# Performance work log

Measured on AMD Instinct MI355X. Metric: run time of the kernel, lower is better.

## Reference

```python
import jax, jax.numpy as jnp
import numpy as np

N_SRC, N_DST = 1000, 1000
N = N_SRC + N_DST          # 2000 == feat_in of SW MLP (hard-coded in original)
D = 128                    # metapath2vec embedding dim
H = 256                    # SW hidden width
B = 100000                 # skip-gram (center, context) pairs
K = 5                      # negatives per pair
EP = 200000                # positive-graph edges
EN = 200000                # negative-graph edges


def setup_inputs() -> dict:
    key = jax.random.key(0)
    ks = jax.random.split(key, 12)
    node_embed = jax.random.normal(ks[0], (N, D), jnp.float32) * 0.1
    context_embed = jax.random.normal(ks[1], (N, D), jnp.float32) * 0.1
    # symmetric bipartite adjacency: etype plus its reverse asetype, homogenized
    A = (jax.random.uniform(ks[2], (N_SRC, N_DST)) < 0.02).astype(jnp.float32)
    adj = jnp.block([[jnp.zeros((N_SRC, N_SRC), jnp.float32), A],
                     [A.T, jnp.zeros((N_DST, N_DST), jnp.float32)]])
    W1 = jax.random.normal(ks[3], (N, H), jnp.float32) / np.sqrt(N).astype(np.float32)
    b1 = jnp.zeros((H,), jnp.float32)
    W2 = jax.random.normal(ks[4], (H, D), jnp.float32) / np.sqrt(H).astype(np.float32)
    b2 = jnp.zeros((D,), jnp.float32)
    pos_u = jax.random.randint(ks[5], (B,), 0, N)
    pos_v = jax.random.randint(ks[6], (B,), 0, N)
    neg_v = jax.random.randint(ks[7], (B, K), 0, N)
    pos_src = jax.random.randint(ks[8], (EP,), 0, N_SRC)
    pos_dst = jax.random.randint(ks[9], (EP,), 0, N_DST)
    neg_src = jax.random.randint(ks[10], (EN,), 0, N_SRC)
    neg_dst = jax.random.randint(ks[11], (EN,), 0, N_DST)
    return dict(node_embed=node_embed, context_embed=context_embed, adj=adj,
                W1=W1, b1=b1, W2=W2, b2=b2,
                pos_u=pos_u, pos_v=pos_v, neg_v=neg_v,
                pos_src=pos_src, pos_dst=pos_dst,
                neg_src=neg_src, neg_dst=neg_dst)


def _skipgram_loss(node_embed, context_embed, pos_u, pos_v, neg_v):
    # DGL MetaPath2Vec negative-sampling skip-gram loss
    emb_u = node_embed[pos_u]            # [B, D] gather
    emb_v = context_embed[pos_v]         # [B, D] gather
    pos = jnp.clip(jnp.sum(emb_u * emb_v, axis=-1), -10.0, 10.0)
    pos_loss = -jax.nn.log_sigmoid(pos)
    emb_neg = context_embed[neg_v]       # [B, K, D] gather
    neg = jnp.clip(jnp.einsum('bkd,bd->bk', emb_neg, emb_u), -10.0, 10.0)
    neg_loss = -jnp.sum(jax.nn.log_sigmoid(-neg), axis=-1)
    return jnp.mean(pos_loss + neg_loss)


def _sw_embedding(adj, feats, W1, b1, W2, b2):
    # adj @ adj @ adj * adj  /  outer(diag(adj@adj))  -> L2-row-normalized -> MLP
    A2 = adj @ adj                       # [N, N]
    part1 = (A2 @ adj) * adj             # 3-path counts masked onto existing edges
    d = jnp.diag(A2)                     # [N]
    part2 = d[:, None] * d[None, :]      # outer product of 2-path counts
    ok = part2 > 0
    gamma = jnp.where(ok, part1 / jnp.where(ok, part2, 1.0), 0.0)  # == nan_to_num
    norm = jnp.sqrt(jnp.sum(gamma * gamma, axis=-1, keepdims=True))
    gamma = gamma / jnp.maximum(norm, 1e-12)          # F.normalize(p=2, dim=1)
    sw_h = jnp.tanh(gamma @ W1 + b1) @ W2 + b2        # [N, 128]
    return jnp.concatenate([feats, sw_h], axis=1)     # [N, 256]


def reference(node_embed, context_embed, adj, W1, b1, W2, b2,
              pos_u, pos_v, neg_v, pos_src, pos_dst, neg_src, neg_dst):
    loss = _skipgram_loss(node_embed, context_embed, pos_u, pos_v, neg_v)
    # feats[etype[0]] ++ feats[etype[2]] == full node_embed table in global order
    h = _sw_embedding(adj, node_embed, W1, b1, W2, b2)
    h_src, h_dst = h[:N_SRC], h[N_SRC:]
    # HeteroDotPredictor: u_dot_v per edge -> [E, 1]
    pos_score = jnp.sum(h_src[pos_src] * h_dst[pos_dst], axis=-1, keepdims=True)
    neg_score = jnp.sum(h_src[neg_src] * h_dst[neg_dst], axis=-1, keepdims=True)
    return loss, pos_score, neg_score
```

## Files before the change

### kernel.cpp

```cpp
#include <hip/hip_runtime.h>
#include <hip/hip_bf16.h>

typedef __attribute__((ext_vector_type(8))) short bf16x8;
typedef __attribute__((ext_vector_type(4))) float f32x4;
typedef __attribute__((ext_vector_type(4))) unsigned short u16x4;
typedef unsigned short u16;

#define BATCH 100000
#define EPE 200000

#define OFF_AP    ((size_t)0)
#define OFF_ATP   ((size_t)2097152)
#define OFF_SP    ((size_t)4194304)
#define OFF_T1    ((size_t)6291456)
#define OFF_G     ((size_t)6291456)
#define OFF_GT    ((size_t)10485760)
#define OFF_GNS   ((size_t)14680064)
#define OFF_GNDT  ((size_t)16777216)
#define OFF_W1AT  ((size_t)18874368)
#define OFF_W1BT  ((size_t)19398656)
#define OFF_W2T   ((size_t)19922944)
#define OFF_HID   ((size_t)19988480)
#define OFF_NEP   ((size_t)21037056)
#define OFF_CEP   ((size_t)21561344)
#define OFF_HSRC  ((size_t)22085632)
#define OFF_HDST  ((size_t)22609920)
#define OFF_T2    ((size_t)23134208)
#define OFF_DEGS  ((size_t)27328512)
#define OFF_DEGD  ((size_t)27332608)
#define OFF_PART  ((size_t)27336704)

__device__ __forceinline__ u16 f2b(float f) {
  union { float f; unsigned u; } v; v.f = f;
  unsigned r = v.u + 0x7fffu + ((v.u >> 16) & 1u);
  return (u16)(r >> 16);
}
__device__ __forceinline__ float b2f(u16 h) {
  union { unsigned u; float f; } v; v.u = ((unsigned)h) << 16;
  return v.f;
}

#define AS1C(p) ((const __attribute__((address_space(1))) void*)(p))
#define AS3(p)  ((__attribute__((address_space(3))) void*)(p))

__global__ __launch_bounds__(256) void prep(const float* __restrict__ adj,
    const float* __restrict__ W1, const float* __restrict__ W2,
    const float* __restrict__ ne, const float* __restrict__ ce,
    u16* __restrict__ Ap, u16* __restrict__ ATp,
    u16* __restrict__ W1At, u16* __restrict__ W1Bt, u16* __restrict__ w2t,
    u16* __restrict__ nep, u16* __restrict__ cep,
    u16* __restrict__ hsrcp, u16* __restrict__ hdstp,
    float* __restrict__ degd, float* __restrict__ degs) {
  __shared__ float tile[64][65];
  __shared__ float redf[256];
  __shared__ float4 red4[8][32];
  int b = blockIdx.x;
  int t = threadIdx.x;
  int tx = t & 63, ty = t >> 6;
  if (b < 256) {
    int tr = b >> 4, tc = b & 15;
    int l16 = t & 15, rq = t >> 4;
    #pragma unroll
    for (int p = 0; p < 4; p++) {
      int r = p * 16 + rq;
      int gr = tr * 64 + r, gc0 = tc * 64 + l16 * 4;
      float4 v = {0.f, 0.f, 0.f, 0.f};
      if (gr < 1000 && gc0 < 1000) v = *(const float4*)&adj[(size_t)gr * 2000 + 1000 + gc0];
      u16x4 pk = {f2b(v.x), f2b(v.y), f2b(v.z), f2b(v.w)};
      *(u16x4*)&Ap[(size_t)gr * 1024 + gc0] = pk;
      tile[r][l16 * 4 + 0] = v.x;
      tile[r][l16 * 4 + 1] = v.y;
      tile[r][l16 * 4 + 2] = v.z;
      tile[r][l16 * 4 + 3] = v.w;
    }
    __syncthreads();
    #pragma unroll
    for (int p = 0; p < 16; p++) {
      int r = p * 4 + ty;
      ATp[(size_t)(tc * 64 + r) * 1024 + tr * 64 + tx] = f2b(tile[tx][r]);
    }
  } else if (b < 384) {
    int b2 = b - 256;
    int half = b2 >> 6, rem = b2 & 63;
    int jt = rem >> 2, ht = rem & 3;
    #pragma unroll
    for (int p = 0; p < 16; p++) {
      int r = p * 4 + ty;
      int j = jt * 64 + r;
      tile[r][tx] = (j < 1000) ? W1[(size_t)(half * 1000 + j) * 256 + ht * 64 + tx] : 0.f;
    }
    __syncthreads();
    u16* outp = half ? W1Bt : W1At;
    #pragma unroll
    for (int p = 0; p < 16; p++) {
      int r = p * 4 + ty;
      outp[(size_t)(ht * 64 + r) * 1024 + jt * 64 + tx] = f2b(tile[tx][r]);
    }
  } else if (b < 392) {
    int b3 = b - 384;
    int dt = b3 >> 2, kt = b3 & 3;
    #pragma unroll
    for (int p = 0; p < 16; p++) {
      int r = p * 4 + ty;
      tile[r][tx] = W2[(size_t)(kt * 64 + r) * 128 + dt * 64 + tx];
    }
    __syncthreads();
    #pragma unroll
    for (int p = 0; p < 16; p++) {
      int r = p * 4 + ty;
      w2t[(size_t)(dt * 64 + r) * 256 + kt * 64 + tx] = f2b(tile[tx][r]);
    }
  } else if (b < 648) {
    int idx = (b - 392) * 256 + t;
    int i = idx >> 5, d4 = (idx & 31) * 4;
    float4 nv = {0.f, 0.f, 0.f, 0.f}, cv = {0.f, 0.f, 0.f, 0.f};
    if (i < 2000) {
      nv = *(const float4*)&ne[(size_t)i * 128 + d4];
      cv = *(const float4*)&ce[(size_t)i * 128 + d4];
    }
    u16x4 nb = {f2b(nv.x), f2b(nv.y), f2b(nv.z), f2b(nv.w)};
    u16x4 cb = {f2b(cv.x), f2b(cv.y), f2b(cv.z), f2b(cv.w)};
    u16x4 zz = {0, 0, 0, 0};
    *(u16x4*)&nep[(size_t)i * 128 + d4] = nb;
    *(u16x4*)&cep[(size_t)i * 128 + d4] = cb;
    if (i < 1000)                   *(u16x4*)&hsrcp[(size_t)i * 256 + d4] = nb;
    else if (i < 1024)              *(u16x4*)&hsrcp[(size_t)i * 256 + d4] = zz;
    if (i >= 1000 && i < 2000)      *(u16x4*)&hdstp[(size_t)(i - 1000) * 256 + d4] = nb;
    else if (i >= 2000 && i < 2024) *(u16x4*)&hdstp[(size_t)(i - 1000) * 256 + d4] = zz;
  } else if (b < 656) {
    int jb = b - 648;
    int cx = t & 31, ry = t >> 5;
    int j4 = jb * 128 + cx * 4;
    float4 s = {0.f, 0.f, 0.f, 0.f};
    if (j4 < 1000)
      for (int i = ry; i < 1000; i += 8) {
        float4 v = *(const float4*)&adj[(size_t)i * 2000 + 1000 + j4];
        s.x += v.x; s.y += v.y; s.z += v.z; s.w += v.w;
      }
    red4[ry][cx] = s;
    __syncthreads();
    if (ry == 0) {
      float4 tot = {0.f, 0.f, 0.f, 0.f};
      #pragma unroll
      for (int k = 0; k < 8; k++) {
        float4 v = red4[k][cx];
        tot.x += v.x; tot.y += v.y; tot.z += v.z; tot.w += v.w;
      }
      *(float4*)&degd[j4] = tot;
    }
  } else {
    int ib = b - 656;
    int r = t >> 3, c8 = t & 7;
    int i = ib * 32 + r;
    float s = 0.f;
    if (i < 1000)
      for (int k4 = c8 * 4; k4 < 1000; k4 += 32) {
        float4 v = *(const float4*)&adj[(size_t)i * 2000 + 1000 + k4];
        s += v.x + v.y + v.z + v.w;
      }
    redf[t] = s;
    __syncthreads();
    if (c8 == 0) {
      float tot = 0.f;
      #pragma unroll
      for (int k = 0; k < 8; k++) tot += redf[r * 8 + k];
      degs[i] = (i < 1000) ? tot : 0.f;
    }
  }
}

__device__ __forceinline__ f32x4 gemm_core32(const u16* __restrict__ A, const u16* __restrict__ BT,
    int K, int lda, int ldbt, int brow, int bcol, u16* As, u16* Bs) {
  const int t = threadIdx.x;
  const int w = t >> 6, lane = t & 63;
  const int wr = w >> 1, wc = w & 1;
  const int r16 = lane & 15, kg = lane >> 4;
  const int row = t >> 3, cc = t & 7;
  f32x4 acc = {0.f, 0.f, 0.f, 0.f};
  const int nst = K >> 6;
  {
    const u16* ga = A + (size_t)(brow + row) * lda + cc * 8;
    __builtin_amdgcn_global_load_lds(AS1C(ga), AS3(As + t * 8), 16, 0, 0);
    const u16* gb = BT + (size_t)(bcol + row) * ldbt + cc * 8;
    __builtin_amdgcn_global_load_lds(AS1C(gb), AS3(Bs + t * 8), 16, 0, 0);
  }
  int cur = 0;
  for (int s = 0; s < nst; ++s) {
    __syncthreads();
    if (s + 1 < nst) {
      int k0 = (s + 1) << 6, nb = cur ^ 1;
      const u16* ga = A + (size_t)(brow + row) * lda + k0 + cc * 8;
      __builtin_amdgcn_global_load_lds(AS1C(ga), AS3(As + nb * 2048 + t * 8), 16, 0, 0);
      const u16* gb = BT + (size_t)(bcol + row) * ldbt + k0 + cc * 8;
      __builtin_amdgcn_global_load_lds(AS1C(gb), AS3(Bs + nb * 2048 + t * 8), 16, 0, 0);
    }
    const u16* Asc = As + cur * 2048;
    const u16* Bsc = Bs + cur * 2048;
    #pragma unroll
    for (int kk = 0; kk < 2; ++kk) {
      bf16x8 af = *(const bf16x8*)&Asc[(wr * 16 + r16) * 64 + kk * 32 + kg * 8];
      bf16x8 bf_ = *(const bf16x8*)&Bsc[(wc * 16 + r16) * 64 + kk * 32 + kg * 8];
      acc = __builtin_amdgcn_mfma_f32_16x16x32_bf16(af, bf_, acc, 0, 0, 0);
    }
    cur ^= 1;
  }
  return acc;
}

__global__ __launch_bounds__(256) void mega1(const u16* __restrict__ nep, const u16* __restrict__ cep,
    const u16* __restrict__ Ap, u16* __restrict__ T1, u16* __restrict__ Sp) {
  __shared__ u16 As[2 * 2048];
  __shared__ u16 Bs[2 * 2048];
  __shared__ u16 mir[32][33];
  int b = blockIdx.x;
  const int t = threadIdx.x;
  const int w = t >> 6, lane = t & 63;
  const int wr = w >> 1, wc = w & 1;
  const int r16 = lane & 15, kg = lane >> 4;
  if (b < 4096) {
    int brow = (b >> 6) * 32, bcol = (b & 63) * 32;
    f32x4 acc = gemm_core32(nep, cep, 128, 128, 128, brow, bcol, As, Bs);
    #pragma unroll
    for (int j = 0; j < 4; j++) {
      int row = brow + wr * 16 + kg * 4 + j, col = bcol + wc * 16 + r16;
      T1[(size_t)row * 2048 + col] = f2b(acc[j]);
    }
  } else {
    int s = b - 4096;
    int bi = (int)((sqrtf(8.f * s + 1.f) - 1.f) * 0.5f);
    while (bi * (bi + 1) / 2 > s) bi--;
    while ((bi + 1) * (bi + 2) / 2 <= s) bi++;
    int bj = s - bi * (bi + 1) / 2;
    int brow = bi * 32, bcol = bj * 32;
    f32x4 acc = gemm_core32(Ap, Ap, 1024, 1024, 1024, brow, bcol, As, Bs);
    #pragma unroll
    for (int j = 0; j < 4; j++) {
      int lr = wr * 16 + kg * 4 + j, lc = wc * 16 + r16;
      u16 v = f2b(acc[j]);
      Sp[(size_t)(brow + lr) * 1024 + bcol + lc] = v;
      mir[lr][lc] = v;
    }
    __syncthreads();
    #pragma unroll
    for (int p = 0; p < 4; p++) {
      int idx = p * 256 + t, rr = idx >> 5, cc2 = idx & 31;
      Sp[(size_t)(bcol + rr) * 1024 + brow + cc2] = mir[cc2][rr];
    }
  }
}

__global__ __launch_bounds__(256) void mega2(const u16* __restrict__ Sp, const u16* __restrict__ ATp,
    const u16* __restrict__ Ap, const float* __restrict__ degs, const float* __restrict__ degd,
    float* __restrict__ G, float* __restrict__ Gt,
    const u16* __restrict__ T1, const int* __restrict__ pu, const int* __restrict__ pv,
    const int* __restrict__ nv, float* __restrict__ partial) {
  __shared__ u16 As[2 * 2048];
  __shared__ u16 Bs[2 * 2048];
  __shared__ float gtile[32][33];
  __shared__ float red[256];
  int b = blockIdx.x;
  const int t = threadIdx.x;
  if (b >= 1024) {
    int s = (b - 1024) * 256 + t;
    float loss = 0.f;
    if (s < BATCH) {
      const u16* trow = T1 + (size_t)pu[s] * 2048;
      const int* nvb = nv + (size_t)s * 5;
      float ap = b2f(trow[pv[s]]);
      ap = fminf(fmaxf(ap, -10.f), 10.f); loss = log1pf(expf(-ap));
      #pragma unroll
      for (int k = 0; k < 5; k++) {
        float a = b2f(trow[nvb[k]]);
        a = fminf(fmaxf(a, -10.f), 10.f);
        loss += log1pf(expf(a));
      }
    }
    red[t] = loss;
    __syncthreads();
    for (int off = 128; off > 0; off >>= 1) {
      if (t < off) red[t] += red[t + off];
      __syncthreads();
    }
    if (t == 0) partial[b - 1024] = red[0];
    return;
  }
  const int w = t >> 6, lane = t & 63;
  const int wr = w >> 1, wc = w & 1;
  const int r16 = lane & 15, kg = lane >> 4;
  int brow = (b >> 5) * 32, bcol = (b & 31) * 32;
  f32x4 acc = gemm_core32(Sp, ATp, 1024, 1024, 1024, brow, bcol, As, Bs);
  #pragma unroll
  for (int j = 0; j < 4; j++) {
    int lr = wr * 16 + kg * 4 + j, lc = wc * 16 + r16;
    int row = brow + lr, col = bcol + lc;
    float a = b2f(Ap[(size_t)row * 1024 + col]);
    float p2 = degs[row] * degd[col];
    float g = (p2 > 0.f) ? (acc[j] * a) / p2 : 0.f;
    G[(size_t)row * 1024 + col] = g;
    gtile[lr][lc] = g;
  }
  __syncthreads();
  #pragma unroll
  for (int p = 0; p < 4; p++) {
    int idx = p * 256 + t, rr = idx >> 5, cc2 = idx & 31;
    Gt[(size_t)(bcol + rr) * 1024 + brow + cc2] = gtile[cc2][rr];
  }
}

template <int EPI>
__global__ __launch_bounds__(256) void gemm_bt(
    const u16* __restrict__ A, const u16* __restrict__ BT,
    const u16* __restrict__ A2, const u16* __restrict__ BT2,
    int K, int lda, int ldbt,
    u16* __restrict__ outb,
    float* __restrict__ outf, int ldo,
    const float* __restrict__ bias,
    u16* __restrict__ hsrcp, u16* __restrict__ hdstp)
{
  __shared__ u16 As[2 * 2048];
  __shared__ u16 Bs[2 * 2048];
  const int t = threadIdx.x;
  const int w = t >> 6, lane = t & 63;
  const int wr = w >> 1, wc = w & 1;
  const int r16 = lane & 15, kg = lane >> 4;
  const int brow = blockIdx.x * 32, bcol = blockIdx.y * 32;
  const u16* Au = (blockIdx.z == 0) ? A : A2;
  const u16* Bu = (blockIdx.z == 0) ? BT : BT2;
  f32x4 acc = gemm_core32(Au, Bu, K, lda, ldbt, brow, bcol, As, Bs);
  #pragma unroll
  for (int j = 0; j < 4; j++) {
    int row = brow + wr * 16 + kg * 4 + j;
    int col = bcol + wc * 16 + r16;
    float val = acc[j];
    if constexpr (EPI == 2) {
      outb[(size_t)(blockIdx.z * 1024 + row) * 256 + col] = f2b(tanhf(val + bias[col]));
    } else if constexpr (EPI == 3) {
      u16 hv = f2b(val + bias[col]);
      if (row < 1024) hsrcp[(size_t)row * 256 + 128 + col] = hv;
      else            hdstp[(size_t)(row - 1024) * 256 + 128 + col] = hv;
    } else {
      outf[(size_t)row * ldo + col] = val;
    }
  }
}

__global__ __launch_bounds__(256) void normk(const float* __restrict__ G, const float* __restrict__ Gt,
                                             u16* __restrict__ Gns, u16* __restrict__ Gndt) {
  __shared__ float red[256];
  int b = blockIdx.x;
  const float* src = (b < 1024) ? (G + (size_t)b * 1024) : (Gt + (size_t)(b - 1024) * 1024);
  u16* dst = (b < 1024) ? (Gns + (size_t)b * 1024) : (Gndt + (size_t)(b - 1024) * 1024);
  float v[4];
  float s = 0.f;
  #pragma unroll
  for (int c = 0; c < 4; c++) { v[c] = src[threadIdx.x + 256 * c]; s += v[c] * v[c]; }
  red[threadIdx.x] = s;
  __syncthreads();
  for (int off = 128; off > 0; off >>= 1) {
    if (threadIdx.x < off) red[threadIdx.x] += red[threadIdx.x + off];
    __syncthreads();
  }
  float inv = 1.0f / fmaxf(sqrtf(red[0]), 1e-12f);
  #pragma unroll
  for (int c = 0; c < 4; c++) dst[threadIdx.x + 256 * c] = f2b(v[c] * inv);
}

__global__ __launch_bounds__(256) void edge_loss(const float* __restrict__ T2,
    const float* __restrict__ partial,
    const int* __restrict__ ps, const int* __restrict__ pd,
    const int* __restrict__ ns, const int* __restrict__ nd,
    float* __restrict__ out) {
  if (blockIdx.x == 1563) {
    __shared__ float red[256];
    float s = 0.f;
    for (int i = threadIdx.x; i < 391; i += 256) s += partial[i];
    red[threadIdx.x] = s;
    __syncthreads();
    for (int off = 128; off > 0; off >>= 1) {
      if (threadIdx.x < off) red[threadIdx.x] += red[threadIdx.x + off];
      __syncthreads();
    }
    if (threadIdx.x == 0) out[0] = red[0] / (float)BATCH;
    return;
  }
  int e = blockIdx.x * 256 + threadIdx.x;
  if (e >= 2 * EPE) return;
  int src, dst;
  if (e < EPE) { src = ps[e]; dst = pd[e]; }
  else         { src = ns[e - EPE]; dst = nd[e - EPE]; }
  out[1 + e] = T2[(size_t)src * 1024 + dst];
}

extern "C" void kernel_launch(void* const* d_in, const int* in_sizes, int n_in,
                              void* d_out, int out_size, void* d_ws, size_t ws_size,
                              hipStream_t stream) {
  const float* node_embed    = (const float*)d_in[0];
  const float* context_embed = (const float*)d_in[1];
  const float* adj           = (const float*)d_in[2];
  const float* W1            = (const float*)d_in[3];
  const float* b1            = (const float*)d_in[4];
  const float* W2            = (const float*)d_in[5];
  const float* b2            = (const float*)d_in[6];
  const int* pos_u   = (const int*)d_in[7];
  const int* pos_v   = (const int*)d_in[8];
  const int* neg_v   = (const int*)d_in[9];
  const int* pos_src = (const int*)d_in[10];
  const int* pos_dst = (const int*)d_in[11];
  const int* neg_src = (const int*)d_in[12];
  const int* neg_dst = (const int*)d_in[13];
  float* out = (float*)d_out;

  char* ws = (char*)d_ws;
  u16*   Ap    = (u16*)(ws + OFF_AP);
  u16*   ATp   = (u16*)(ws + OFF_ATP);
  u16*   Sp    = (u16*)(ws + OFF_SP);
  u16*   T1    = (u16*)(ws + OFF_T1);
  float* G     = (float*)(ws + OFF_G);
  float* Gt    = (float*)(ws + OFF_GT);
  u16*   Gns   = (u16*)(ws + OFF_GNS);
  u16*   Gndt  = (u16*)(ws + OFF_GNDT);
  u16*   W1At  = (u16*)(ws + OFF_W1AT);
  u16*   W1Bt  = (u16*)(ws + OFF_W1BT);
  u16*   w2t   = (u16*)(ws + OFF_W2T);
  u16*   hid   = (u16*)(ws + OFF_HID);
  u16*   nep   = (u16*)(ws + OFF_NEP);
  u16*   cep   = (u16*)(ws + OFF_CEP);
  u16*   hsrcp = (u16*)(ws + OFF_HSRC);
  u16*   hdstp = (u16*)(ws + OFF_HDST);
  float* T2    = (float*)(ws + OFF_T2);
  float* degs  = (float*)(ws + OFF_DEGS);
  float* degd  = (float*)(ws + OFF_DEGD);
  float* part  = (float*)(ws + OFF_PART);

  prep<<<688, 256, 0, stream>>>(adj, W1, W2, node_embed, context_embed,
                                Ap, ATp, W1At, W1Bt, w2t, nep, cep, hsrcp, hdstp, degd, degs);

  mega1<<<4624, 256, 0, stream>>>(nep, cep, Ap, T1, Sp);

  mega2<<<1415, 256, 0, stream>>>(Sp, ATp, Ap, degs, degd, G, Gt,
                                  T1, pos_u, pos_v, neg_v, part);

  normk<<<2048, 256, 0, stream>>>(G, Gt, Gns, Gndt);

  gemm_bt<2><<<dim3(32, 8, 2), 256, 0, stream>>>(Gns, W1Bt, Gndt, W1At, 1024, 1024, 1024,
      hid, nullptr, 0, b1, nullptr, nullptr);

  gemm_bt<3><<<dim3(64, 4), 256, 0, stream>>>(hid, w2t, nullptr, nullptr, 256, 256, 256,
      nullptr, nullptr, 0, b2, hsrcp, hdstp);

  gemm_bt<4><<<dim3(32, 32), 256, 0, stream>>>(hsrcp, hdstp, nullptr, nullptr, 256, 256, 256,
      nullptr, T2, 1024, nullptr, nullptr, nullptr);

  edge_loss<<<1564, 256, 0, stream>>>(T2, part, pos_src, pos_dst, neg_src, neg_dst, out);
}
```

Baseline: 111.7 us.

## Enlarge GEMM tiles to 64x64 with XOR-swizzled LDS staging

Replaces the 32x32-per-block GEMM core with a 64x64 core in which each wave computes a 2x2 grid of 16x16 MFMA tiles, staging operands through LDS with an XOR swizzle to avoid bank conflicts. All GEMM kernels (mega1, mega2, and the new dedicated hid/w2/t2 kernels) use the larger tiles, which cuts block counts and increases operand reuse per load. T1 and G no longer share workspace, so the offsets are remapped. The trade-off is fewer blocks for the small GEMMs (64 to 256), which may underfill the GPU, plus more register and LDS use per block.

```diff
diff --git a/kernel.cpp b/kernel.cpp
--- a/kernel.cpp
+++ b/kernel.cpp
@@ -13,22 +13,22 @@
 #define OFF_ATP   ((size_t)2097152)
 #define OFF_SP    ((size_t)4194304)
 #define OFF_T1    ((size_t)6291456)
-#define OFF_G     ((size_t)6291456)
-#define OFF_GT    ((size_t)10485760)
-#define OFF_GNS   ((size_t)14680064)
-#define OFF_GNDT  ((size_t)16777216)
-#define OFF_W1AT  ((size_t)18874368)
-#define OFF_W1BT  ((size_t)19398656)
-#define OFF_W2T   ((size_t)19922944)
-#define OFF_HID   ((size_t)19988480)
-#define OFF_NEP   ((size_t)21037056)
-#define OFF_CEP   ((size_t)21561344)
-#define OFF_HSRC  ((size_t)22085632)
-#define OFF_HDST  ((size_t)22609920)
-#define OFF_T2    ((size_t)23134208)
-#define OFF_DEGS  ((size_t)27328512)
-#define OFF_DEGD  ((size_t)27332608)
-#define OFF_PART  ((size_t)27336704)
+#define OFF_G     ((size_t)14680064)
+#define OFF_GT    ((size_t)18874368)
+#define OFF_GNS   ((size_t)23068672)
+#define OFF_GNDT  ((size_t)25165824)
+#define OFF_W1AT  ((size_t)27262976)
+#define OFF_W1BT  ((size_t)27787264)
+#define OFF_W2T   ((size_t)28311552)
+#define OFF_HID   ((size_t)28377088)
+#define OFF_NEP   ((size_t)29425664)
+#define OFF_CEP   ((size_t)29950208)
+#define OFF_HSRC  ((size_t)30474752)
+#define OFF_HDST  ((size_t)30999296)
+#define OFF_T2    ((size_t)31523840)
+#define OFF_DEGS  ((size_t)35718144)
+#define OFF_DEGD  ((size_t)35722240)
+#define OFF_PART  ((size_t)35726336)
 
 __device__ __forceinline__ u16 f2b(float f) {
   union { float f; unsigned u; } v; v.f = f;
@@ -113,13 +113,13 @@
   } else if (b < 648) {
     int idx = (b - 392) * 256 + t;
     int i = idx >> 5, d4 = (idx & 31) * 4;
-    float4 nv = {0.f, 0.f, 0.f, 0.f}, cv = {0.f, 0.f, 0.f, 0.f};
+    float4 nv4 = {0.f, 0.f, 0.f, 0.f}, cv4 = {0.f, 0.f, 0.f, 0.f};
     if (i < 2000) {
-      nv = *(const float4*)&ne[(size_t)i * 128 + d4];
-      cv = *(const float4*)&ce[(size_t)i * 128 + d4];
-    }
-    u16x4 nb = {f2b(nv.x), f2b(nv.y), f2b(nv.z), f2b(nv.w)};
-    u16x4 cb = {f2b(cv.x), f2b(cv.y), f2b(cv.z), f2b(cv.w)};
+      nv4 = *(const float4*)&ne[(size_t)i * 128 + d4];
+      cv4 = *(const float4*)&ce[(size_t)i * 128 + d4];
+    }
+    u16x4 nb = {f2b(nv4.x), f2b(nv4.y), f2b(nv4.z), f2b(nv4.w)};
+    u16x4 cb = {f2b(cv4.x), f2b(cv4.y), f2b(cv4.z), f2b(cv4.w)};
     u16x4 zz = {0, 0, 0, 0};
     *(u16x4*)&nep[(size_t)i * 128 + d4] = nb;
     *(u16x4*)&cep[(size_t)i * 128 + d4] = cb;
@@ -169,38 +169,59 @@
   }
 }
 
-__device__ __forceinline__ f32x4 gemm_core32(const u16* __restrict__ A, const u16* __restrict__ BT,
+struct Acc22 { f32x4 a[2][2]; };
+__device__ __forceinline__ Acc22 gemm_core64(const u16* A, const u16* BT,
     int K, int lda, int ldbt, int brow, int bcol, u16* As, u16* Bs) {
   const int t = threadIdx.x;
   const int w = t >> 6, lane = t & 63;
   const int wr = w >> 1, wc = w & 1;
   const int r16 = lane & 15, kg = lane >> 4;
-  const int row = t >> 3, cc = t & 7;
-  f32x4 acc = {0.f, 0.f, 0.f, 0.f};
+  Acc22 acc;
+  #pragma unroll
+  for (int m = 0; m < 2; m++)
+    #pragma unroll
+    for (int n = 0; n < 2; n++) {
+      f32x4 z = {0.f, 0.f, 0.f, 0.f};
+      acc.a[m][n] = z;
+    }
+  auto stage = [&](u16* dA, u16* dB, int k0) {
+    #pragma unroll
+    for (int it = 0; it < 2; ++it) {
+      int chunk = it * 256 + t;
+      int row = chunk >> 3, c = (chunk & 7) ^ (row & 7);
+      const u16* ga = A + (size_t)(brow + row) * lda + k0 + c * 8;
+      __builtin_amdgcn_global_load_lds(AS1C(ga), AS3(dA + chunk * 8), 16, 0, 0);
+      const u16* gb = BT + (size_t)(bcol + row) * ldbt + k0 + c * 8;
+      __builtin_amdgcn_global_load_lds(AS1C(gb), AS3(dB + chunk * 8), 16, 0, 0);
+    }
+  };
   const int nst = K >> 6;
-  {
-    const u16* ga = A + (size_t)(brow + row) * lda + cc * 8;
-    __builtin_amdgcn_global_load_lds(AS1C(ga), AS3(As + t * 8), 16, 0, 0);
-    const u16* gb = BT + (size_t)(bcol + row) * ldbt + cc * 8;
-    __builtin_amdgcn_global_load_lds(AS1C(gb), AS3(Bs + t * 8), 16, 0, 0);
-  }
+  stage(As, Bs, 0);
   int cur = 0;
   for (int s = 0; s < nst; ++s) {
     __syncthreads();
-    if (s + 1 < nst) {
-      int k0 = (s + 1) << 6, nb = cur ^ 1;
-      const u16* ga = A + (size_t)(brow + row) * lda + k0 + cc * 8;
-      __builtin_amdgcn_global_load_lds(AS1C(ga), AS3(As + nb * 2048 + t * 8), 16, 0, 0);
-      const u16* gb = BT + (size_t)(bcol + row) * ldbt + k0 + cc * 8;
-      __builtin_amdgcn_global_load_lds(AS1C(gb), AS3(Bs + nb * 2048 + t * 8), 16, 0, 0);
-    }
-    const u16* Asc = As + cur * 2048;
-    const u16* Bsc = Bs + cur * 2048;
+    if (s + 1 < nst) stage(As + (cur ^ 1) * 4096, Bs + (cur ^ 1) * 4096, (s + 1) << 6);
+    const u16* Asc = As + cur * 4096;
+    const u16* Bsc = Bs + cur * 4096;
     #pragma unroll
     for (int kk = 0; kk < 2; ++kk) {
-      bf16x8 af = *(const bf16x8*)&Asc[(wr * 16 + r16) * 64 + kk * 32 + kg * 8];
-      bf16x8 bf_ = *(const bf16x8*)&Bsc[(wc * 16 + r16) * 64 + kk * 32 + kg * 8];
-      acc = __builtin_amdgcn_mfma_f32_16x16x32_bf16(af, bf_, acc, 0, 0, 0);
+      int g = kk * 4 + kg;
+      bf16x8 af[2], bfr[2];
+      #pragma unroll
+      for (int m = 0; m < 2; m++) {
+        int Ra = wr * 32 + m * 16 + r16;
+        af[m] = *(const bf16x8*)&Asc[Ra * 64 + ((g ^ (Ra & 7)) * 8)];
+      }
+      #pragma unroll
+      for (int n = 0; n < 2; n++) {
+        int Rb = wc * 32 + n * 16 + r16;
+        bfr[n] = *(const bf16x8*)&Bsc[Rb * 64 + ((g ^ (Rb & 7)) * 8)];
+      }
+      #pragma unroll
+      for (int m = 0; m < 2; m++)
+        #pragma unroll
+        for (int n = 0; n < 2; n++)
+          acc.a[m][n] = __builtin_amdgcn_mfma_f32_16x16x32_bf16(af[m], bfr[n], acc.a[m][n], 0, 0, 0);
     }
     cur ^= 1;
   }
@@ -209,42 +230,52 @@
 
 __global__ __launch_bounds__(256) void mega1(const u16* __restrict__ nep, const u16* __restrict__ cep,
     const u16* __restrict__ Ap, u16* __restrict__ T1, u16* __restrict__ Sp) {
-  __shared__ u16 As[2 * 2048];
-  __shared__ u16 Bs[2 * 2048];
-  __shared__ u16 mir[32][33];
+  __shared__ u16 As[2 * 4096];
+  __shared__ u16 Bs[2 * 4096];
+  __shared__ u16 mir[64 * 65];
   int b = blockIdx.x;
   const int t = threadIdx.x;
   const int w = t >> 6, lane = t & 63;
   const int wr = w >> 1, wc = w & 1;
   const int r16 = lane & 15, kg = lane >> 4;
-  if (b < 4096) {
-    int brow = (b >> 6) * 32, bcol = (b & 63) * 32;
-    f32x4 acc = gemm_core32(nep, cep, 128, 128, 128, brow, bcol, As, Bs);
-    #pragma unroll
-    for (int j = 0; j < 4; j++) {
-      int row = brow + wr * 16 + kg * 4 + j, col = bcol + wc * 16 + r16;
-      T1[(size_t)row * 2048 + col] = f2b(acc[j]);
-    }
+  if (b < 1024) {
+    int brow = (b >> 5) * 64, bcol = (b & 31) * 64;
+    Acc22 acc = gemm_core64(nep, cep, 128, 128, 128, brow, bcol, As, Bs);
+    #pragma unroll
+    for (int m = 0; m < 2; m++)
+      #pragma unroll
+      for (int n = 0; n < 2; n++)
+        #pragma unroll
+        for (int j = 0; j < 4; j++) {
+          int row = brow + wr * 32 + m * 16 + kg * 4 + j;
+          int col = bcol + wc * 32 + n * 16 + r16;
+          T1[(size_t)row * 2048 + col] = f2b(acc.a[m][n][j]);
+        }
   } else {
-    int s = b - 4096;
+    int s = b - 1024;
     int bi = (int)((sqrtf(8.f * s + 1.f) - 1.f) * 0.5f);
     while (bi * (bi + 1) / 2 > s) bi--;
     while ((bi + 1) * (bi + 2) / 2 <= s) bi++;
     int bj = s - bi * (bi + 1) / 2;
-    int brow = bi * 32, bcol = bj * 32;
-    f32x4 acc = gemm_core32(Ap, Ap, 1024, 1024, 1024, brow, bcol, As, Bs);
-    #pragma unroll
-    for (int j = 0; j < 4; j++) {
-      int lr = wr * 16 + kg * 4 + j, lc = wc * 16 + r16;
-      u16 v = f2b(acc[j]);
-      Sp[(size_t)(brow + lr) * 1024 + bcol + lc] = v;
-      mir[lr][lc] = v;
-    }
-    __syncthreads();
-    #pragma unroll
-    for (int p = 0; p < 4; p++) {
-      int idx = p * 256 + t, rr = idx >> 5, cc2 = idx & 31;
-      Sp[(size_t)(bcol + rr) * 1024 + brow + cc2] = mir[cc2][rr];
+    int brow = bi * 64, bcol = bj * 64;
+    Acc22 acc = gemm_core64(Ap, Ap, 1024, 1024, 1024, brow, bcol, As, Bs);
+    #pragma unroll
+    for (int m = 0; m < 2; m++)
+      #pragma unroll
+      for (int n = 0; n < 2; n++)
+        #pragma unroll
+        for (int j = 0; j < 4; j++) {
+          int lr = wr * 32 + m * 16 + kg * 4 + j;
+          int lc = wc * 32 + n * 16 + r16;
+          u16 v = f2b(acc.a[m][n][j]);
+          Sp[(size_t)(brow + lr) * 1024 + bcol + lc] = v;
+          mir[lr * 65 + lc] = v;
+        }
+    __syncthreads();
+    #pragma unroll
+    for (int p = 0; p < 16; p++) {
+      int idx = p * 256 + t, rr = idx >> 6, cc = idx & 63;
+      Sp[(size_t)(bcol + rr) * 1024 + brow + cc] = mir[cc * 65 + rr];
     }
   }
 }
@@ -254,14 +285,15 @@
     float* __restrict__ G, float* __restrict__ Gt,
     const u16* __restrict__ T1, const int* __restrict__ pu, const int* __restrict__ pv,
     const int* __restrict__ nv, float* __restrict__ partial) {
-  __shared__ u16 As[2 * 2048];
-  __shared__ u16 Bs[2 * 2048];
-  __shared__ float gtile[32][33];
-  __shared__ float red[256];
+  __shared__ char sm[49664] __attribute__((aligned(16)));
+  u16* As = (u16*)sm;
+  u16* Bs = (u16*)(sm + 16384);
+  float* gtile = (float*)(sm + 32768);
+  float* red = (float*)sm;
   int b = blockIdx.x;
   const int t = threadIdx.x;
-  if (b >= 1024) {
-    int s = (b - 1024) * 256 + t;
+  if (b >= 256) {
+    int s = (b - 256) * 256 + t;
     float loss = 0.f;
     if (s < BATCH) {
       const u16* trow = T1 + (size_t)pu[s] * 2048;
@@ -281,66 +313,34 @@
       if (t < off) red[t] += red[t + off];
       __syncthreads();
     }
-    if (t == 0) partial[b - 1024] = red[0];
+    if (t == 0) partial[b - 256] = red[0];
     return;
   }
   const int w = t >> 6, lane = t & 63;
   const int wr = w >> 1, wc = w & 1;
   const int r16 = lane & 15, kg = lane >> 4;
-  int brow = (b >> 5) * 32, bcol = (b & 31) * 32;
-  f32x4 acc = gemm_core32(Sp, ATp, 1024, 1024, 1024, brow, bcol, As, Bs);
-  #pragma unroll
-  for (int j = 0; j < 4; j++) {
-    int lr = wr * 16 + kg * 4 + j, lc = wc * 16 + r16;
-    int row = brow + lr, col = bcol + lc;
-    float a = b2f(Ap[(size_t)row * 1024 + col]);
-    float p2 = degs[row] * degd[col];
-    float g = (p2 > 0.f) ? (acc[j] * a) / p2 : 0.f;
-    G[(size_t)row * 1024 + col] = g;
-    gtile[lr][lc] = g;
-  }
+  int brow = (b >> 4) * 64, bcol = (b & 15) * 64;
+  Acc22 acc = gemm_core64(Sp, ATp, 1024, 1024, 1024, brow, bcol, As, Bs);
+  #pragma unroll
+  for (int m = 0; m < 2; m++)
+    #pragma unroll
+    for (int n = 0; n < 2; n++)
+      #pragma unroll
+      for (int j = 0; j < 4; j++) {
+        int lr = wr * 32 + m * 16 + kg * 4 + j;
+        int lc = wc * 32 + n * 16 + r16;
+        int row = brow + lr, col = bcol + lc;
+        float a = b2f(Ap[(size_t)row * 1024 + col]);
+        float p2 = degs[row] * degd[col];
+        float g = (p2 > 0.f) ? (acc.a[m][n][j] * a) / p2 : 0.f;
+        G[(size_t)row * 1024 + col] = g;
+        gtile[lr * 65 + lc] = g;
+      }
   __syncthreads();
   #pragma unroll
-  for (int p = 0; p < 4; p++) {
-    int idx = p * 256 + t, rr = idx >> 5, cc2 = idx & 31;
-    Gt[(size_t)(bcol + rr) * 1024 + brow + cc2] = gtile[cc2][rr];
-  }
-}
-
-template <int EPI>
-__global__ __launch_bounds__(256) void gemm_bt(
-    const u16* __restrict__ A, const u16* __restrict__ BT,
-    const u16* __restrict__ A2, const u16* __restrict__ BT2,
-    int K, int lda, int ldbt,
-    u16* __restrict__ outb,
-    float* __restrict__ outf, int ldo,
-    const float* __restrict__ bias,
-    u16* __restrict__ hsrcp, u16* __restrict__ hdstp)
-{
-  __shared__ u16 As[2 * 2048];
-  __shared__ u16 Bs[2 * 2048];
-  const int t = threadIdx.x;
-  const int w = t >> 6, lane = t & 63;
-  const int wr = w >> 1, wc = w & 1;
-  const int r16 = lane & 15, kg = lane >> 4;
-  const int brow = blockIdx.x * 32, bcol = blockIdx.y * 32;
-  const u16* Au = (blockIdx.z == 0) ? A : A2;
-  const u16* Bu = (blockIdx.z == 0) ? BT : BT2;
-  f32x4 acc = gemm_core32(Au, Bu, K, lda, ldbt, brow, bcol, As, Bs);
-  #pragma unroll
-  for (int j = 0; j < 4; j++) {
-    int row = brow + wr * 16 + kg * 4 + j;
-    int col = bcol + wc * 16 + r16;
-    float val = acc[j];
-    if constexpr (EPI == 2) {
-      outb[(size_t)(blockIdx.z * 1024 + row) * 256 + col] = f2b(tanhf(val + bias[col]));
-    } else if constexpr (EPI == 3) {
-      u16 hv = f2b(val + bias[col]);
-      if (row < 1024) hsrcp[(size_t)row * 256 + 128 + col] = hv;
-      else            hdstp[(size_t)(row - 1024) * 256 + 128 + col] = hv;
-    } else {
-      outf[(size_t)row * ldo + col] = val;
-    }
+  for (int p = 0; p < 16; p++) {
+    int idx = p * 256 + t, rr = idx >> 6, cc = idx & 63;
+    Gt[(size_t)(bcol + rr) * 1024 + brow + cc] = gtile[cc * 65 + rr];
   }
 }
 
@@ -363,6 +363,81 @@
   float inv = 1.0f / fmaxf(sqrtf(red[0]), 1e-12f);
   #pragma unroll
   for (int c = 0; c < 4; c++) dst[threadIdx.x + 256 * c] = f2b(v[c] * inv);
+}
+
+__global__ __launch_bounds__(256) void gemm_hid(const u16* __restrict__ Gns, const u16* __restrict__ W1Bt,
+    const u16* __restrict__ Gndt, const u16* __restrict__ W1At,
+    const float* __restrict__ b1, u16* __restrict__ hid) {
+  __shared__ u16 As[2 * 4096];
+  __shared__ u16 Bs[2 * 4096];
+  const int t = threadIdx.x;
+  const int w = t >> 6, lane = t & 63;
+  const int wr = w >> 1, wc = w & 1;
+  const int r16 = lane & 15, kg = lane >> 4;
+  int b = blockIdx.x;
+  int z = b >> 6, rem = b & 63;
+  int brow = (rem & 15) * 64, bcol = (rem >> 4) * 64;
+  const u16* Au = z ? Gndt : Gns;
+  const u16* Bu = z ? W1At : W1Bt;
+  Acc22 acc = gemm_core64(Au, Bu, 1024, 1024, 1024, brow, bcol, As, Bs);
+  #pragma unroll
+  for (int m = 0; m < 2; m++)
+    #pragma unroll
+    for (int n = 0; n < 2; n++)
+      #pragma unroll
+      for (int j = 0; j < 4; j++) {
+        int row = brow + wr * 32 + m * 16 + kg * 4 + j;
+        int col = bcol + wc * 32 + n * 16 + r16;
+        hid[(size_t)((z << 10) + row) * 256 + col] = f2b(tanhf(acc.a[m][n][j] + b1[col]));
+      }
+}
+
+__global__ __launch_bounds__(256) void gemm_w2(const u16* __restrict__ hid, const u16* __restrict__ w2t,
+    const float* __restrict__ b2, u16* __restrict__ hsrcp, u16* __restrict__ hdstp) {
+  __shared__ u16 As[2 * 4096];
+  __shared__ u16 Bs[2 * 4096];
+  const int t = threadIdx.x;
+  const int w = t >> 6, lane = t & 63;
+  const int wr = w >> 1, wc = w & 1;
+  const int r16 = lane & 15, kg = lane >> 4;
+  int b = blockIdx.x;
+  int brow = (b >> 1) * 64, bcol = (b & 1) * 64;
+  Acc22 acc = gemm_core64(hid, w2t, 256, 256, 256, brow, bcol, As, Bs);
+  #pragma unroll
+  for (int m = 0; m < 2; m++)
+    #pragma unroll
+    for (int n = 0; n < 2; n++)
+      #pragma unroll
+      for (int j = 0; j < 4; j++) {
+        int row = brow + wr * 32 + m * 16 + kg * 4 + j;
+        int col = bcol + wc * 32 + n * 16 + r16;
+        u16 hv = f2b(acc.a[m][n][j] + b2[col]);
+        if (row < 1024) hsrcp[(size_t)row * 256 + 128 + col] = hv;
+        else            hdstp[(size_t)(row - 1024) * 256 + 128 + col] = hv;
+      }
+}
+
+__global__ __launch_bounds__(256) void gemm_t2(const u16* __restrict__ hsrcp, const u16* __restrict__ hdstp,
+    float* __restrict__ T2) {
+  __shared__ u16 As[2 * 4096];
+  __shared__ u16 Bs[2 * 4096];
+  const int t = threadIdx.x;
+  const int w = t >> 6, lane = t & 63;
+  const int wr = w >> 1, wc = w & 1;
+  const int r16 = lane & 15, kg = lane >> 4;
+  int b = blockIdx.x;
+  int brow = (b >> 4) * 64, bcol = (b & 15) * 64;
+  Acc22 acc = gemm_core64(hsrcp, hdstp, 256, 256, 256, brow, bcol, As, Bs);
+  #pragma unroll
+  for (int m = 0; m < 2; m++)
+    #pragma unroll
+    for (int n = 0; n < 2; n++)
+      #pragma unroll
+      for (int j = 0; j < 4; j++) {
+        int row = brow + wr * 32 + m * 16 + kg * 4 + j;
+        int col = bcol + wc * 32 + n * 16 + r16;
+        T2[(size_t)row * 1024 + col] = acc.a[m][n][j];
+      }
 }
 
 __global__ __launch_bounds__(256) void edge_loss(const float* __restrict__ T2,
@@ -434,22 +509,11 @@
 
   prep<<<688, 256, 0, stream>>>(adj, W1, W2, node_embed, context_embed,
                                 Ap, ATp, W1At, W1Bt, w2t, nep, cep, hsrcp, hdstp, degd, degs);
-
-  mega1<<<4624, 256, 0, stream>>>(nep, cep, Ap, T1, Sp);
-
-  mega2<<<1415, 256, 0, stream>>>(Sp, ATp, Ap, degs, degd, G, Gt,
-                                  T1, pos_u, pos_v, neg_v, part);
-
+  mega1<<<1160, 256, 0, stream>>>(nep, cep, Ap, T1, Sp);
+  mega2<<<647, 256, 0, stream>>>(Sp, ATp, Ap, degs, degd, G, Gt, T1, pos_u, pos_v, neg_v, part);
   normk<<<2048, 256, 0, stream>>>(G, Gt, Gns, Gndt);
-
-  gemm_bt<2><<<dim3(32, 8, 2), 256, 0, stream>>>(Gns, W1Bt, Gndt, W1At, 1024, 1024, 1024,
-      hid, nullptr, 0, b1, nullptr, nullptr);
-
-  gemm_bt<3><<<dim3(64, 4), 256, 0, stream>>>(hid, w2t, nullptr, nullptr, 256, 256, 256,
-      nullptr, nullptr, 0, b2, hsrcp, hdstp);
-
-  gemm_bt<4><<<dim3(32, 32), 256, 0, stream>>>(hsrcp, hdstp, nullptr, nullptr, 256, 256, 256,
-      nullptr, T2, 1024, nullptr, nullptr, nullptr);
-
+  gemm_hid<<<128, 256, 0, stream>>>(Gns, W1Bt, Gndt, W1At, b1, hid);
+  gemm_w2<<<64, 256, 0, stream>>>(hid, w2t, b2, hsrcp, hdstp);
+  gemm_t2<<<256, 256, 0, stream>>>(hsrcp, hdstp, T2);
   edge_loss<<<1564, 256, 0, stream>>>(T2, part, pos_src, pos_dst, neg_src, neg_dst, out);
 }
```

Result: slower. 117.7 us (+5.4%).

## Fuse row normalization into GEMM epilogue, swizzle LDS, reorder mega1 blocks

Applied to the files above, without the earlier changes.

Removes the separate normalization kernel and the fp32 G/Gt intermediates. mega2 now writes unnormalized bf16 gamma directly and emits per-tile partial sums of squares. The hidden-layer GEMM reduces those partials and applies the inverse row norm in its epilogue. The shared GEMM core also gains an XOR swizzle on LDS chunk placement to cut bank conflicts. mega1 now schedules the longer triangular Ap·Apᵀ blocks before the short embedding blocks. The trade-off is that gamma is rounded to bf16 before normalization rather than after, which slightly changes numerics.

```diff
diff --git a/kernel.cpp b/kernel.cpp
--- a/kernel.cpp
+++ b/kernel.cpp
@@ -13,8 +13,6 @@
 #define OFF_ATP   ((size_t)2097152)
 #define OFF_SP    ((size_t)4194304)
 #define OFF_T1    ((size_t)6291456)
-#define OFF_G     ((size_t)6291456)
-#define OFF_GT    ((size_t)10485760)
 #define OFF_GNS   ((size_t)14680064)
 #define OFF_GNDT  ((size_t)16777216)
 #define OFF_W1AT  ((size_t)18874368)
@@ -26,9 +24,11 @@
 #define OFF_HSRC  ((size_t)22085632)
 #define OFF_HDST  ((size_t)22609920)
 #define OFF_T2    ((size_t)23134208)
-#define OFF_DEGS  ((size_t)27328512)
-#define OFF_DEGD  ((size_t)27332608)
-#define OFF_PART  ((size_t)27336704)
+#define OFF_ROWP  ((size_t)27328512)
+#define OFF_COLP  ((size_t)27459584)
+#define OFF_DEGS  ((size_t)27590656)
+#define OFF_DEGD  ((size_t)27594752)
+#define OFF_PART  ((size_t)27598848)
 
 __device__ __forceinline__ u16 f2b(float f) {
   union { float f; unsigned u; } v; v.f = f;
@@ -113,13 +113,13 @@
   } else if (b < 648) {
     int idx = (b - 392) * 256 + t;
     int i = idx >> 5, d4 = (idx & 31) * 4;
-    float4 nv = {0.f, 0.f, 0.f, 0.f}, cv = {0.f, 0.f, 0.f, 0.f};
+    float4 nv4 = {0.f, 0.f, 0.f, 0.f}, cv4 = {0.f, 0.f, 0.f, 0.f};
     if (i < 2000) {
-      nv = *(const float4*)&ne[(size_t)i * 128 + d4];
-      cv = *(const float4*)&ce[(size_t)i * 128 + d4];
-    }
-    u16x4 nb = {f2b(nv.x), f2b(nv.y), f2b(nv.z), f2b(nv.w)};
-    u16x4 cb = {f2b(cv.x), f2b(cv.y), f2b(cv.z), f2b(cv.w)};
+      nv4 = *(const float4*)&ne[(size_t)i * 128 + d4];
+      cv4 = *(const float4*)&ce[(size_t)i * 128 + d4];
+    }
+    u16x4 nb = {f2b(nv4.x), f2b(nv4.y), f2b(nv4.z), f2b(nv4.w)};
+    u16x4 cb = {f2b(cv4.x), f2b(cv4.y), f2b(cv4.z), f2b(cv4.w)};
     u16x4 zz = {0, 0, 0, 0};
     *(u16x4*)&nep[(size_t)i * 128 + d4] = nb;
     *(u16x4*)&cep[(size_t)i * 128 + d4] = cb;
@@ -169,37 +169,41 @@
   }
 }
 
-__device__ __forceinline__ f32x4 gemm_core32(const u16* __restrict__ A, const u16* __restrict__ BT,
+__device__ __forceinline__ f32x4 gemm_core32(const u16* A, const u16* BT,
     int K, int lda, int ldbt, int brow, int bcol, u16* As, u16* Bs) {
   const int t = threadIdx.x;
   const int w = t >> 6, lane = t & 63;
   const int wr = w >> 1, wc = w & 1;
   const int r16 = lane & 15, kg = lane >> 4;
-  const int row = t >> 3, cc = t & 7;
+  const int row = t >> 3;
+  const int csrc = (t & 7) ^ (row & 7);
   f32x4 acc = {0.f, 0.f, 0.f, 0.f};
   const int nst = K >> 6;
   {
-    const u16* ga = A + (size_t)(brow + row) * lda + cc * 8;
+    const u16* ga = A + (size_t)(brow + row) * lda + csrc * 8;
     __builtin_amdgcn_global_load_lds(AS1C(ga), AS3(As + t * 8), 16, 0, 0);
-    const u16* gb = BT + (size_t)(bcol + row) * ldbt + cc * 8;
+    const u16* gb = BT + (size_t)(bcol + row) * ldbt + csrc * 8;
     __builtin_amdgcn_global_load_lds(AS1C(gb), AS3(Bs + t * 8), 16, 0, 0);
   }
+  const int Ra = wr * 16 + r16;
+  const int Rb = wc * 16 + r16;
   int cur = 0;
   for (int s = 0; s < nst; ++s) {
     __syncthreads();
     if (s + 1 < nst) {
       int k0 = (s + 1) << 6, nb = cur ^ 1;
-      const u16* ga = A + (size_t)(brow + row) * lda + k0 + cc * 8;
+      const u16* ga = A + (size_t)(brow + row) * lda + k0 + csrc * 8;
       __builtin_amdgcn_global_load_lds(AS1C(ga), AS3(As + nb * 2048 + t * 8), 16, 0, 0);
-      const u16* gb = BT + (size_t)(bcol + row) * ldbt + k0 + cc * 8;
+      const u16* gb = BT + (size_t)(bcol + row) * ldbt + k0 + csrc * 8;
       __builtin_amdgcn_global_load_lds(AS1C(gb), AS3(Bs + nb * 2048 + t * 8), 16, 0, 0);
     }
     const u16* Asc = As + cur * 2048;
     const u16* Bsc = Bs + cur * 2048;
     #pragma unroll
     for (int kk = 0; kk < 2; ++kk) {
-      bf16x8 af = *(const bf16x8*)&Asc[(wr * 16 + r16) * 64 + kk * 32 + kg * 8];
-      bf16x8 bf_ = *(const bf16x8*)&Bsc[(wc * 16 + r16) * 64 + kk * 32 + kg * 8];
+      int g = kk * 4 + kg;
+      bf16x8 af = *(const bf16x8*)&Asc[Ra * 64 + ((g ^ (Ra & 7)) * 8)];
+      bf16x8 bf_ = *(const bf16x8*)&Bsc[Rb * 64 + ((g ^ (Rb & 7)) * 8)];
       acc = __builtin_amdgcn_mfma_f32_16x16x32_bf16(af, bf_, acc, 0, 0, 0);
     }
     cur ^= 1;
@@ -211,22 +215,14 @@
     const u16* __restrict__ Ap, u16* __restrict__ T1, u16* __restrict__ Sp) {
   __shared__ u16 As[2 * 2048];
   __shared__ u16 Bs[2 * 2048];
-  __shared__ u16 mir[32][33];
-  int b = blockIdx.x;
-  const int t = threadIdx.x;
-  const int w = t >> 6, lane = t & 63;
-  const int wr = w >> 1, wc = w & 1;
-  const int r16 = lane & 15, kg = lane >> 4;
-  if (b < 4096) {
-    int brow = (b >> 6) * 32, bcol = (b & 63) * 32;
-    f32x4 acc = gemm_core32(nep, cep, 128, 128, 128, brow, bcol, As, Bs);
-    #pragma unroll
-    for (int j = 0; j < 4; j++) {
-      int row = brow + wr * 16 + kg * 4 + j, col = bcol + wc * 16 + r16;
-      T1[(size_t)row * 2048 + col] = f2b(acc[j]);
-    }
-  } else {
-    int s = b - 4096;
+  __shared__ u16 mir[32 * 33];
+  int b = blockIdx.x;
+  const int t = threadIdx.x;
+  const int w = t >> 6, lane = t & 63;
+  const int wr = w >> 1, wc = w & 1;
+  const int r16 = lane & 15, kg = lane >> 4;
+  if (b < 528) {
+    int s = b;
     int bi = (int)((sqrtf(8.f * s + 1.f) - 1.f) * 0.5f);
     while (bi * (bi + 1) / 2 > s) bi--;
     while ((bi + 1) * (bi + 2) / 2 <= s) bi++;
@@ -238,25 +234,35 @@
       int lr = wr * 16 + kg * 4 + j, lc = wc * 16 + r16;
       u16 v = f2b(acc[j]);
       Sp[(size_t)(brow + lr) * 1024 + bcol + lc] = v;
-      mir[lr][lc] = v;
+      mir[lr * 33 + lc] = v;
     }
     __syncthreads();
     #pragma unroll
     for (int p = 0; p < 4; p++) {
-      int idx = p * 256 + t, rr = idx >> 5, cc2 = idx & 31;
-      Sp[(size_t)(bcol + rr) * 1024 + brow + cc2] = mir[cc2][rr];
+      int idx = p * 256 + t, rr = idx >> 5, cc = idx & 31;
+      Sp[(size_t)(bcol + rr) * 1024 + brow + cc] = mir[cc * 33 + rr];
+    }
+  } else {
+    int b2 = b - 528;
+    int brow = (b2 >> 6) * 32, bcol = (b2 & 63) * 32;
+    f32x4 acc = gemm_core32(nep, cep, 128, 128, 128, brow, bcol, As, Bs);
+    #pragma unroll
+    for (int j = 0; j < 4; j++) {
+      int row = brow + wr * 16 + kg * 4 + j, col = bcol + wc * 16 + r16;
+      T1[(size_t)row * 2048 + col] = f2b(acc[j]);
     }
   }
 }
 
 __global__ __launch_bounds__(256) void mega2(const u16* __restrict__ Sp, const u16* __restrict__ ATp,
     const u16* __restrict__ Ap, const float* __restrict__ degs, const float* __restrict__ degd,
-    float* __restrict__ G, float* __restrict__ Gt,
+    u16* __restrict__ Gns, u16* __restrict__ Gndt,
+    float* __restrict__ rowp, float* __restrict__ colp,
     const u16* __restrict__ T1, const int* __restrict__ pu, const int* __restrict__ pv,
     const int* __restrict__ nv, float* __restrict__ partial) {
   __shared__ u16 As[2 * 2048];
   __shared__ u16 Bs[2 * 2048];
-  __shared__ float gtile[32][33];
+  __shared__ float gtile[32 * 33];
   __shared__ float red[256];
   int b = blockIdx.x;
   const int t = threadIdx.x;
@@ -296,73 +302,100 @@
     float a = b2f(Ap[(size_t)row * 1024 + col]);
     float p2 = degs[row] * degd[col];
     float g = (p2 > 0.f) ? (acc[j] * a) / p2 : 0.f;
-    G[(size_t)row * 1024 + col] = g;
-    gtile[lr][lc] = g;
+    Gns[(size_t)row * 1024 + col] = f2b(g);
+    gtile[lr * 33 + lc] = g;
   }
   __syncthreads();
   #pragma unroll
   for (int p = 0; p < 4; p++) {
-    int idx = p * 256 + t, rr = idx >> 5, cc2 = idx & 31;
-    Gt[(size_t)(bcol + rr) * 1024 + brow + cc2] = gtile[cc2][rr];
-  }
-}
-
-template <int EPI>
-__global__ __launch_bounds__(256) void gemm_bt(
-    const u16* __restrict__ A, const u16* __restrict__ BT,
-    const u16* __restrict__ A2, const u16* __restrict__ BT2,
-    int K, int lda, int ldbt,
-    u16* __restrict__ outb,
-    float* __restrict__ outf, int ldo,
-    const float* __restrict__ bias,
-    u16* __restrict__ hsrcp, u16* __restrict__ hdstp)
-{
+    int idx = p * 256 + t, rr = idx >> 5, cc = idx & 31;
+    Gndt[(size_t)(bcol + rr) * 1024 + brow + cc] = f2b(gtile[cc * 33 + rr]);
+  }
+  if (t < 32) {
+    float s = 0.f;
+    #pragma unroll
+    for (int k = 0; k < 32; k++) { float g = gtile[t * 33 + k]; s += g * g; }
+    rowp[(size_t)(bcol >> 5) * 1024 + brow + t] = s;
+  } else if (t < 64) {
+    int c = t - 32;
+    float s = 0.f;
+    #pragma unroll
+    for (int k = 0; k < 32; k++) { float g = gtile[k * 33 + c]; s += g * g; }
+    colp[(size_t)(brow >> 5) * 1024 + bcol + c] = s;
+  }
+}
+
+__global__ __launch_bounds__(256) void gemm_hid(const u16* __restrict__ Gns, const u16* __restrict__ W1Bt,
+    const u16* __restrict__ Gndt, const u16* __restrict__ W1At,
+    const float* __restrict__ rowp, const float* __restrict__ colp,
+    const float* __restrict__ b1, u16* __restrict__ hid) {
   __shared__ u16 As[2 * 2048];
   __shared__ u16 Bs[2 * 2048];
-  const int t = threadIdx.x;
-  const int w = t >> 6, lane = t & 63;
-  const int wr = w >> 1, wc = w & 1;
-  const int r16 = lane & 15, kg = lane >> 4;
-  const int brow = blockIdx.x * 32, bcol = blockIdx.y * 32;
-  const u16* Au = (blockIdx.z == 0) ? A : A2;
-  const u16* Bu = (blockIdx.z == 0) ? BT : BT2;
-  f32x4 acc = gemm_core32(Au, Bu, K, lda, ldbt, brow, bcol, As, Bs);
+  __shared__ float invr[32];
+  const int t = threadIdx.x;
+  const int w = t >> 6, lane = t & 63;
+  const int wr = w >> 1, wc = w & 1;
+  const int r16 = lane & 15, kg = lane >> 4;
+  int b = blockIdx.x;
+  int z = b >> 8, rem = b & 255;
+  int brow = (rem & 31) * 32, bcol = (rem >> 5) * 32;
+  if (t < 32) {
+    const float* pp = z ? colp : rowp;
+    float s = 0.f;
+    #pragma unroll
+    for (int k = 0; k < 32; k++) s += pp[(size_t)k * 1024 + brow + t];
+    invr[t] = 1.0f / fmaxf(sqrtf(s), 1e-12f);
+  }
+  const u16* Au = z ? Gndt : Gns;
+  const u16* Bu = z ? W1At : W1Bt;
+  f32x4 acc = gemm_core32(Au, Bu, 1024, 1024, 1024, brow, bcol, As, Bs);
+  #pragma unroll
+  for (int j = 0; j < 4; j++) {
+    int lr = wr * 16 + kg * 4 + j;
+    int row = brow + lr;
+    int col = bcol + wc * 16 + r16;
+    hid[(size_t)((z << 10) + row) * 256 + col] = f2b(tanhf(acc[j] * invr[lr] + b1[col]));
+  }
+}
+
+__global__ __launch_bounds__(256) void gemm_w2(const u16* __restrict__ hid, const u16* __restrict__ w2t,
+    const float* __restrict__ b2, u16* __restrict__ hsrcp, u16* __restrict__ hdstp) {
+  __shared__ u16 As[2 * 2048];
+  __shared__ u16 Bs[2 * 2048];
+  const int t = threadIdx.x;
+  const int w = t >> 6, lane = t & 63;
+  const int wr = w >> 1, wc = w & 1;
+  const int r16 = lane & 15, kg = lane >> 4;
+  int b = blockIdx.x;
+  int brow = (b >> 2) * 32, bcol = (b & 3) * 32;
+  f32x4 acc = gemm_core32(hid, w2t, 256, 256, 256, brow, bcol, As, Bs);
   #pragma unroll
   for (int j = 0; j < 4; j++) {
     int row = brow + wr * 16 + kg * 4 + j;
     int col = bcol + wc * 16 + r16;
-    float val = acc[j];
-    if constexpr (EPI == 2) {
-      outb[(size_t)(blockIdx.z * 1024 + row) * 256 + col] = f2b(tanhf(val + bias[col]));
-    } else if constexpr (EPI == 3) {
-      u16 hv = f2b(val + bias[col]);
-      if (row < 1024) hsrcp[(size_t)row * 256 + 128 + col] = hv;
-      else            hdstp[(size_t)(row - 1024) * 256 + 128 + col] = hv;
-    } else {
-      outf[(size_t)row * ldo + col] = val;
-    }
-  }
-}
-
-__global__ __launch_bounds__(256) void normk(const float* __restrict__ G, const float* __restrict__ Gt,
-                                             u16* __restrict__ Gns, u16* __restrict__ Gndt) {
-  __shared__ float red[256];
-  int b = blockIdx.x;
-  const float* src = (b < 1024) ? (G + (size_t)b * 1024) : (Gt + (size_t)(b - 1024) * 1024);
-  u16* dst = (b < 1024) ? (Gns + (size_t)b * 1024) : (Gndt + (size_t)(b - 1024) * 1024);
-  float v[4];
-  float s = 0.f;
+    u16 hv = f2b(acc[j] + b2[col]);
+    if (row < 1024) hsrcp[(size_t)row * 256 + 128 + col] = hv;
+    else            hdstp[(size_t)(row - 1024) * 256 + 128 + col] = hv;
+  }
+}
+
+__global__ __launch_bounds__(256) void gemm_t2(const u16* __restrict__ hsrcp, const u16* __restrict__ hdstp,
+    float* __restrict__ T2) {
+  __shared__ u16 As[2 * 2048];
+  __shared__ u16 Bs[2 * 2048];
+  const int t = threadIdx.x;
+  const int w = t >> 6, lane = t & 63;
+  const int wr = w >> 1, wc = w & 1;
+  const int r16 = lane & 15, kg = lane >> 4;
+  int b = blockIdx.x;
+  int brow = (b >> 5) * 32, bcol = (b & 31) * 32;
+  f32x4 acc = gemm_core32(hsrcp, hdstp, 256, 256, 256, brow, bcol, As, Bs);
   #pragma unroll
-  for (int c = 0; c < 4; c++) { v[c] = src[threadIdx.x + 256 * c]; s += v[c] * v[c]; }
-  red[threadIdx.x] = s;
-  __syncthreads();
-  for (int off = 128; off > 0; off >>= 1) {
-    if (threadIdx.x < off) red[threadIdx.x] += red[threadIdx.x + off];
-    __syncthreads();
-  }
-  float inv = 1.0f / fmaxf(sqrtf(red[0]), 1e-12f);
-  #pragma unroll
-  for (int c = 0; c < 4; c++) dst[threadIdx.x + 256 * c] = f2b(v[c] * inv);
+  for (int j = 0; j < 4; j++) {
+    int row = brow + wr * 16 + kg * 4 + j;
+    int col = bcol + wc * 16 + r16;
+    T2[(size_t)row * 1024 + col] = acc[j];
+  }
 }
 
 __global__ __launch_bounds__(256) void edge_loss(const float* __restrict__ T2,
@@ -415,8 +448,6 @@
   u16*   ATp   = (u16*)(ws + OFF_ATP);
   u16*   Sp    = (u16*)(ws + OFF_SP);
   u16*   T1    = (u16*)(ws + OFF_T1);
-  float* G     = (float*)(ws + OFF_G);
-  float* Gt    = (float*)(ws + OFF_GT);
   u16*   Gns   = (u16*)(ws + OFF_GNS);
   u16*   Gndt  = (u16*)(ws + OFF_GNDT);
   u16*   W1At  = (u16*)(ws + OFF_W1AT);
@@ -428,28 +459,19 @@
   u16*   hsrcp = (u16*)(ws + OFF_HSRC);
   u16*   hdstp = (u16*)(ws + OFF_HDST);
   float* T2    = (float*)(ws + OFF_T2);
+  float* rowp  = (float*)(ws + OFF_ROWP);
+  float* colp  = (float*)(ws + OFF_COLP);
   float* degs  = (float*)(ws + OFF_DEGS);
   float* degd  = (float*)(ws + OFF_DEGD);
   float* part  = (float*)(ws + OFF_PART);
 
   prep<<<688, 256, 0, stream>>>(adj, W1, W2, node_embed, context_embed,
                                 Ap, ATp, W1At, W1Bt, w2t, nep, cep, hsrcp, hdstp, degd, degs);
-
   mega1<<<4624, 256, 0, stream>>>(nep, cep, Ap, T1, Sp);
-
-  mega2<<<1415, 256, 0, stream>>>(Sp, ATp, Ap, degs, degd, G, Gt,
+  mega2<<<1415, 256, 0, stream>>>(Sp, ATp, Ap, degs, degd, Gns, Gndt, rowp, colp,
                                   T1, pos_u, pos_v, neg_v, part);
-
-  normk<<<2048, 256, 0, stream>>>(G, Gt, Gns, Gndt);
-
-  gemm_bt<2><<<dim3(32, 8, 2), 256, 0, stream>>>(Gns, W1Bt, Gndt, W1At, 1024, 1024, 1024,
-      hid, nullptr, 0, b1, nullptr, nullptr);
-
-  gemm_bt<3><<<dim3(64, 4), 256, 0, stream>>>(hid, w2t, nullptr, nullptr, 256, 256, 256,
-      nullptr, nullptr, 0, b2, hsrcp, hdstp);
-
-  gemm_bt<4><<<dim3(32, 32), 256, 0, stream>>>(hsrcp, hdstp, nullptr, nullptr, 256, 256, 256,
-      nullptr, T2, 1024, nullptr, nullptr, nullptr);
-
+  gemm_hid<<<512, 256, 0, stream>>>(Gns, W1Bt, Gndt, W1At, rowp, colp, b1, hid);
+  gemm_w2<<<256, 256, 0, stream>>>(hid, w2t, b2, hsrcp, hdstp);
+  gemm_t2<<<1024, 256, 0, stream>>>(hsrcp, hdstp, T2);
   edge_loss<<<1564, 256, 0, stream>>>(T2, part, pos_src, pos_dst, neg_src, neg_dst, out);
 }
```

Result: faster. 103.2 us (-7.5%).
